# Kernel tuning notes

Hardware: AMD Instinct MI355X
Metric: run time of the kernel (lower is better)

The kernel has to match this reference:

```python
import jax, jax.numpy as jnp
import numpy as np

MEAN_STOP_TIME_S = 60.0
MIN_ROUTE_LEN = 2
DEMAND_TIME_WEIGHT = 0.5
ROUTE_TIME_WEIGHT = 0.5
UNSERVED_WEIGHT = 5.0

B, N, R, L, K = 64, 512, 40, 20, 4


def setup_inputs() -> dict:
    key = jax.random.key(0)
    ks = jax.random.split(key, 8)
    demand = jax.random.uniform(ks[0], (B, N, N), dtype=jnp.float32) * 10.0
    drive_times = jax.random.uniform(ks[1], (B, N, N), dtype=jnp.float32) * 1800.0
    transit_times = jax.random.uniform(ks[2], (B, N, N), dtype=jnp.float32) * 3600.0
    has_path = jax.random.randint(ks[3], (B, N, N), 0, 2) > 0
    n_transfers = jax.random.randint(ks[4], (B, N, N), 0, 4).astype(jnp.int32)
    # routes with -1 padding past a random per-route length
    routes = jax.random.randint(ks[5], (B, R, L), 0, N).astype(jnp.int32)
    lens = jax.random.randint(ks[6], (B, R), 0, L + 1)
    valid = jnp.arange(L)[None, None, :] < lens[:, :, None]
    batch_routes = jnp.where(valid, routes, -1)
    # per demand-edge route assignments, -1 = unused slot
    route_seqs = (jax.random.randint(ks[7], (B, N, N, K), 0, R + 1) - 1).astype(jnp.int32)
    return {
        'demand': demand, 'drive_times': drive_times, 'transit_times': transit_times,
        'has_path': has_path, 'n_transfers': n_transfers,
        'batch_routes': batch_routes, 'route_seqs': route_seqs,
    }


def _route_leg_times(batch_routes, dtm, mean_stop_time_s):
    # leg (l -> l+1) of each route: dtm[b, from, to] + stop time, masked on valid stops
    frm = batch_routes[:, :, :-1]
    to = batch_routes[:, :, 1:]
    valid = (frm >= 0) & (to >= 0)
    bidx = jnp.arange(dtm.shape[0])[:, None, None]
    times = dtm[bidx, jnp.maximum(frm, 0), jnp.maximum(to, 0)] + mean_stop_time_s
    return jnp.where(valid, times, 0.0)  # [B, R, L-1]


def _per_route_riders(demand, route_seqs, n_routes):
    # segment-sum demand over route ids; -1 slots go to a dump bucket
    def per_b(dem, rs):
        ids = rs.reshape(-1)
        vals = jnp.broadcast_to(dem[..., None], rs.shape).reshape(-1)
        ids = jnp.where(ids < 0, n_routes, ids)
        return jax.ops.segment_sum(vals, ids, num_segments=n_routes + 1)[:n_routes]
    return jax.vmap(per_b)(demand, route_seqs)  # [B, R]


def reference(demand, drive_times, transit_times, has_path, n_transfers,
              batch_routes, route_seqs):
    fdem = demand
    nopath = ~has_path
    route_lens = (batch_routes > -1).sum(-1)  # [B, R]

    n_disconnected = (nopath & (fdem > 0)).sum(axis=(1, 2))
    route_len_delta = jnp.maximum(MIN_ROUTE_LEN - route_lens, 0)
    route_len_delta = jnp.where(route_lens == 0, 0, route_len_delta)
    n_stops_oob = route_len_delta.sum(-1)  # [B]

    nt_eff = jnp.where(nopath, 3, n_transfers)
    tat = jnp.stack([
        (fdem * (nt_eff == 0)).sum(axis=(1, 2)),
        (fdem * (nt_eff == 1)).sum(axis=(1, 2)),
        (fdem * (nt_eff == 2)).sum(axis=(1, 2)),
        (fdem * (nt_eff > 2)).sum(axis=(1, 2)),
    ], axis=-1)  # trips_at_transfers [B, 4]

    trip_times = jnp.where(nopath, 0.0, transit_times)
    total_dmd_time = (fdem * trip_times).sum(axis=(1, 2))
    total_transfers = (fdem * n_transfers.astype(fdem.dtype)).sum(axis=(1, 2))
    unserved = (fdem * nopath).sum(axis=(1, 2))
    total_demand = fdem.sum(axis=(1, 2))

    leg_times = _route_leg_times(batch_routes, drive_times, MEAN_STOP_TIME_S)
    total_route_time = leg_times.sum(axis=(1, 2))
    # symmetric_routes=True: add return-direction legs
    ret = _route_leg_times(batch_routes, jnp.swapaxes(drive_times, 1, 2), MEAN_STOP_TIME_S)
    total_route_time = total_route_time + ret.sum(axis=(1, 2))

    per_route_riders = _per_route_riders(fdem, route_seqs, R)

    # cost assembly
    time_norm = drive_times.max(axis=(1, 2))
    served = total_demand - unserved
    mean_dmd_time = total_dmd_time / (served + 1e-6)
    norm_dmd_time = mean_dmd_time / time_norm
    n_routes_used = (route_lens > 0).sum(-1)
    norm_route_time = total_route_time / (time_norm * n_routes_used + 1e-6)
    n_demand_edges = (fdem > 0).sum(axis=(1, 2))
    frac_uncovered = n_disconnected / n_demand_edges
    denom = n_routes_used * MIN_ROUTE_LEN
    frac_oob = n_stops_oob / (denom + 1e-6)
    cost = (DEMAND_TIME_WEIGHT * norm_dmd_time
            + ROUTE_TIME_WEIGHT * norm_route_time
            + UNSERVED_WEIGHT * (frac_uncovered + frac_oob))
    return cost, per_route_riders, tat, total_route_time


if __name__ == '__main__':
    out = reference(**setup_inputs())
    print([o.shape for o in out])
```

## Files before the change

kernel.cpp:

```cpp
#include <hip/hip_runtime.h>

#define NB 64
#define NDIM 512
#define NNE (NDIM * NDIM)
#define NR 40
#define NL 20
#define SUBS 16
#define IT 16
#define BINS 41

#define MAIN_STRIDE 64
#define RT_OFF (NB * SUBS * MAIN_STRIDE)
#define FLAG_OFF (RT_OFF + NB * 4)

__global__ void detect_kernel(const unsigned int* __restrict__ hp, int* __restrict__ flag) {
    unsigned int v = hp[threadIdx.x];
    unsigned long long m = __ballot(v > 1u);
    if (threadIdx.x == 0) *flag = (m != 0ull) ? 1 : 0;
}

template<bool BYTE>
__device__ __forceinline__ void mloop(
    const float* __restrict__ pd, const float* __restrict__ pt,
    const float* __restrict__ pdr, const int* __restrict__ pn,
    const void* __restrict__ ph, const int* __restrict__ pr,
    float acc[10], float* __restrict__ myrow)
{
#pragma unroll 2
    for (int it = 0; it < IT; ++it) {
        const int o = it * 1024;
        const float4 dem = *(const float4*)(pd + o);
        const float4 tt  = *(const float4*)(pt + o);
        const float4 dt  = *(const float4*)(pdr + o);
        const int4   nt  = *(const int4*)(pn + o);
        const int4 r0 = *(const int4*)(pr + o * 4);
        const int4 r1 = *(const int4*)(pr + o * 4 + 4);
        const int4 r2 = *(const int4*)(pr + o * 4 + 8);
        const int4 r3 = *(const int4*)(pr + o * 4 + 12);
        int h[4];
        if (BYTE) {
            const uchar4 hb = *(const uchar4*)((const unsigned char*)ph + o);
            h[0] = hb.x; h[1] = hb.y; h[2] = hb.z; h[3] = hb.w;
        } else {
            const int4 hw = *(const int4*)((const int*)ph + o);
            h[0] = hw.x; h[1] = hw.y; h[2] = hw.z; h[3] = hw.w;
        }
        const float dm[4] = {dem.x, dem.y, dem.z, dem.w};
        const float tv[4] = {tt.x, tt.y, tt.z, tt.w};
        const float dv[4] = {dt.x, dt.y, dt.z, dt.w};
        const int   nv[4] = {nt.x, nt.y, nt.z, nt.w};
        const int4  rr[4] = {r0, r1, r2, r3};
#pragma unroll
        for (int e = 0; e < 4; ++e) {
            const float d = dm[e];
            const bool np_ = (h[e] == 0);
            const int nte = np_ ? 3 : nv[e];
            acc[0] += (nte == 0) ? d : 0.0f;
            acc[1] += (nte == 1) ? d : 0.0f;
            acc[2] += (nte == 2) ? d : 0.0f;
            acc[3] += (nte > 2) ? d : 0.0f;
            acc[4] += np_ ? 0.0f : d * tv[e];
            acc[5] += np_ ? d : 0.0f;
            acc[6] += d;
            const bool pos = d > 0.0f;
            acc[7] += (np_ && pos) ? 1.0f : 0.0f;
            acc[8] += pos ? 1.0f : 0.0f;
            acc[9] = fmaxf(acc[9], dv[e]);

            const unsigned b0 = min((unsigned)rr[e].x, (unsigned)(BINS - 1));
            const unsigned b1 = min((unsigned)rr[e].y, (unsigned)(BINS - 1));
            const unsigned b2 = min((unsigned)rr[e].z, (unsigned)(BINS - 1));
            const unsigned b3 = min((unsigned)rr[e].w, (unsigned)(BINS - 1));
            const float a0 = d;
            const float a1 = d * (1.0f + (b1 == b0));
            const float a2 = d * (1.0f + (b2 == b0) + (b2 == b1));
            const float a3 = d * (1.0f + (b3 == b0) + (b3 == b1) + (b3 == b2));
            const float v0 = myrow[b0];
            const float v1 = myrow[b1];
            const float v2 = myrow[b2];
            const float v3 = myrow[b3];
            myrow[b0] = v0 + a0;
            myrow[b1] = v1 + a1;
            myrow[b2] = v2 + a2;
            myrow[b3] = v3 + a3;
        }
    }
}

__global__ __launch_bounds__(256, 3) void main_kernel(
    const float* __restrict__ demand,
    const float* __restrict__ transit,
    const float* __restrict__ drive,
    const int* __restrict__ ntr,
    const unsigned char* __restrict__ hp_raw,
    const int* __restrict__ rseq,
    const int* __restrict__ flag,
    float* __restrict__ ws)
{
    __shared__ float bins[256 * BINS];
    __shared__ float red[4][10];
    __shared__ float red2[4][NR];
    const int tid = threadIdx.x;
    const int wave = tid >> 6, lane = tid & 63;
    float* __restrict__ myrow = bins + tid * BINS;
#pragma unroll
    for (int i = 0; i < BINS; ++i) myrow[i] = 0.0f;

    const int b = blockIdx.x >> 4, sub = blockIdx.x & 15;
    const size_t e0 = (size_t)b * NNE + (size_t)sub * (NNE / SUBS) + (size_t)tid * 4;

    float acc[10] = {0, 0, 0, 0, 0, 0, 0, 0, 0, 0};
    if (*flag != 0)
        mloop<true>(demand + e0, transit + e0, drive + e0, ntr + e0,
                    hp_raw + e0, rseq + e0 * 4, acc, myrow);
    else
        mloop<false>(demand + e0, transit + e0, drive + e0, ntr + e0,
                     ((const int*)hp_raw) + e0, rseq + e0 * 4, acc, myrow);

#pragma unroll
    for (int o = 32; o > 0; o >>= 1) {
#pragma unroll
        for (int v = 0; v < 9; ++v) acc[v] += __shfl_down(acc[v], o);
        acc[9] = fmaxf(acc[9], __shfl_down(acc[9], o));
    }
    if (lane == 0)
#pragma unroll
        for (int v = 0; v < 10; ++v) red[wave][v] = acc[v];
    __syncthreads();

    float* part = ws + (size_t)blockIdx.x * MAIN_STRIDE;
    if (tid < 10) {
        if (tid == 9)
            part[9] = fmaxf(fmaxf(red[0][9], red[1][9]), fmaxf(red[2][9], red[3][9]));
        else
            part[tid] = red[0][tid] + red[1][tid] + red[2][tid] + red[3][tid];
    }

    if (tid < 4 * NR) {
        const int g = tid / NR, j = tid - g * NR;
        float s = 0.0f;
#pragma unroll 8
        for (int r = g * 64; r < g * 64 + 64; ++r) s += bins[r * BINS + j];
        red2[g][j] = s;
    }
    __syncthreads();
    if (tid < NR)
        part[10 + tid] = red2[0][tid] + red2[1][tid] + red2[2][tid] + red2[3][tid];
}

__global__ __launch_bounds__(64) void route_kernel(
    const int* __restrict__ routes,
    const float* __restrict__ drive,
    float* __restrict__ ws)
{
    const int b = blockIdx.x;
    const int r = threadIdx.x;
    float t = 0.0f, used = 0.0f, oob = 0.0f;
    if (r < NR) {
        const int* rt = routes + (b * NR + r) * NL;
        int v[NL];
        int len = 0;
#pragma unroll
        for (int l = 0; l < NL; ++l) { v[l] = rt[l]; len += (v[l] > -1) ? 1 : 0; }
        const float* D = drive + (size_t)b * NNE;
#pragma unroll
        for (int l = 0; l < NL - 1; ++l) {
            int f = v[l], to = v[l + 1];
            if (f >= 0 && to >= 0)
                t += D[f * NDIM + to] + D[to * NDIM + f] + 120.0f;
        }
        used = (len > 0) ? 1.0f : 0.0f;
        int delta = 2 - len;
        oob = (len > 0 && delta > 0) ? (float)delta : 0.0f;
    }
#pragma unroll
    for (int o = 32; o > 0; o >>= 1) {
        t += __shfl_down(t, o);
        used += __shfl_down(used, o);
        oob += __shfl_down(oob, o);
    }
    if (r == 0) {
        float* a = ws + RT_OFF + b * 4;
        a[0] = t; a[1] = used; a[2] = oob;
    }
}

__global__ __launch_bounds__(64) void final_kernel(const float* __restrict__ ws,
                                                   float* __restrict__ out) {
    __shared__ float fin[50];
    const int b = blockIdx.x;
    const int v = threadIdx.x;
    if (v < 50) {
        const float* p = ws + (size_t)b * SUBS * MAIN_STRIDE + v;
        float a = p[0];
#pragma unroll
        for (int s = 1; s < SUBS; ++s) {
            const float x = p[(size_t)s * MAIN_STRIDE];
            a = (v == 9) ? fmaxf(a, x) : (a + x);
        }
        fin[v] = a;
    }
    __syncthreads();
    if (v == 0) {
        const float* rt = ws + RT_OFF + b * 4;
        const float trt = rt[0], nru = rt[1], noob = rt[2];
        const float dmdt = fin[4], uns = fin[5], tdem = fin[6];
        const float ndisc = fin[7], nedge = fin[8], tn = fin[9];
        const float served = tdem - uns;
        const float cost = 0.5f * ((dmdt / (served + 1e-6f)) / tn)
                         + 0.5f * (trt / (tn * nru + 1e-6f))
                         + 5.0f * (ndisc / nedge + noob / (nru * 2.0f + 1e-6f));
        out[b] = cost;
        out[64 + NB * NR + NB * 4 + b] = trt;
    }
    if (v < 4) out[64 + NB * NR + b * 4 + v] = fin[v];
    if (v >= 10 && v < 50) out[64 + b * NR + (v - 10)] = fin[v];
}

extern "C" void kernel_launch(void* const* d_in, const int* in_sizes, int n_in,
                              void* d_out, int out_size, void* d_ws, size_t ws_size,
                              hipStream_t stream) {
    const float* demand  = (const float*)d_in[0];
    const float* drive   = (const float*)d_in[1];
    const float* transit = (const float*)d_in[2];
    const unsigned char* hp = (const unsigned char*)d_in[3];
    const int* ntr    = (const int*)d_in[4];
    const int* routes = (const int*)d_in[5];
    const int* rseq   = (const int*)d_in[6];
    float* out = (float*)d_out;
    float* ws  = (float*)d_ws;
    int* flag  = (int*)(ws + FLAG_OFF);

    detect_kernel<<<1, 64, 0, stream>>>((const unsigned int*)hp, flag);
    route_kernel<<<NB, 64, 0, stream>>>(routes, drive, ws);
    main_kernel<<<NB * SUBS, 256, 0, stream>>>(demand, transit, drive, ntr, hp, rseq, flag, ws);
    final_kernel<<<NB, 64, 0, stream>>>(ws, out);
}
```

Baseline: 133.8 us.

## Software-pipeline main loop, shrink histogram LDS, merge route kernel into final

The main loop now double-buffers global loads in register structs, so the next group's loads are in flight while the current group is processed. The shared histogram drops the dump bin (40 bins instead of 41, invalid ids are weighted to zero) and occupancy is raised to 4 blocks per CU. The in-block cross-wave reductions and second barrier are removed: per-wave partials go straight to the workspace and the final kernel sums them. The route-time kernel is folded into the final kernel, saving one launch. Costs are higher register pressure from the double buffer, a 40-stride LDS layout that may raise bank conflicts, and a larger final reduction.

```diff
diff --git a/kernel.cpp b/kernel.cpp
--- a/kernel.cpp
+++ b/kernel.cpp
@@ -7,16 +7,97 @@
 #define NL 20
 #define SUBS 16
 #define IT 16
-#define BINS 41
-
-#define MAIN_STRIDE 64
-#define RT_OFF (NB * SUBS * MAIN_STRIDE)
-#define FLAG_OFF (RT_OFF + NB * 4)
+
+#define MAIN_STRIDE 256
+#define FLAG_OFF (NB * SUBS * MAIN_STRIDE)
+#define OUT_RIDERS 64
+#define OUT_TAT (64 + NB * NR)
+#define OUT_TRT (64 + NB * NR + NB * 4)
 
 __global__ void detect_kernel(const unsigned int* __restrict__ hp, int* __restrict__ flag) {
     unsigned int v = hp[threadIdx.x];
     unsigned long long m = __ballot(v > 1u);
     if (threadIdx.x == 0) *flag = (m != 0ull) ? 1 : 0;
+}
+
+struct G {
+    float4 dem, tt, dt;
+    int4 nt, r0, r1, r2, r3;
+    int h0, h1, h2, h3;
+};
+
+template<bool BYTE>
+__device__ __forceinline__ void ld(G& g,
+    const float* __restrict__ pd, const float* __restrict__ pt,
+    const float* __restrict__ pdr, const int* __restrict__ pn,
+    const void* __restrict__ ph, const int* __restrict__ pr, int o)
+{
+    g.dem = *(const float4*)(pd + o);
+    g.tt  = *(const float4*)(pt + o);
+    g.dt  = *(const float4*)(pdr + o);
+    g.nt  = *(const int4*)(pn + o);
+    g.r0  = *(const int4*)(pr + o * 4);
+    g.r1  = *(const int4*)(pr + o * 4 + 4);
+    g.r2  = *(const int4*)(pr + o * 4 + 8);
+    g.r3  = *(const int4*)(pr + o * 4 + 12);
+    if (BYTE) {
+        const uchar4 hb = *(const uchar4*)((const unsigned char*)ph + o);
+        g.h0 = hb.x; g.h1 = hb.y; g.h2 = hb.z; g.h3 = hb.w;
+    } else {
+        const int4 hw = *(const int4*)((const int*)ph + o);
+        g.h0 = hw.x; g.h1 = hw.y; g.h2 = hw.z; g.h3 = hw.w;
+    }
+}
+
+__device__ __forceinline__ void procE(float d, float ttv, float dtv, int ntv, int hv,
+                                      int i0, int i1, int i2, int i3,
+                                      float acc[10], float* __restrict__ myrow)
+{
+    const bool np_ = (hv == 0);
+    const int nte = np_ ? 3 : ntv;
+    acc[0] += (nte == 0) ? d : 0.0f;
+    acc[1] += (nte == 1) ? d : 0.0f;
+    acc[2] += (nte == 2) ? d : 0.0f;
+    acc[3] += (nte > 2) ? d : 0.0f;
+    acc[4] += np_ ? 0.0f : d * ttv;
+    acc[5] += np_ ? d : 0.0f;
+    acc[6] += d;
+    const bool pos = d > 0.0f;
+    acc[7] += (np_ && pos) ? 1.0f : 0.0f;
+    acc[8] += pos ? 1.0f : 0.0f;
+    acc[9] = fmaxf(acc[9], dtv);
+
+    const unsigned u0 = (unsigned)i0, u1 = (unsigned)i1,
+                   u2 = (unsigned)i2, u3 = (unsigned)i3;
+    const unsigned b0 = min(u0, (unsigned)(NR - 1));
+    const unsigned b1 = min(u1, (unsigned)(NR - 1));
+    const unsigned b2 = min(u2, (unsigned)(NR - 1));
+    const unsigned b3 = min(u3, (unsigned)(NR - 1));
+    const float w0 = (u0 < NR) ? d : 0.0f;
+    const float w1 = (u1 < NR) ? d : 0.0f;
+    const float w2 = (u2 < NR) ? d : 0.0f;
+    const float w3 = (u3 < NR) ? d : 0.0f;
+    const float a0 = w0;
+    const float a1 = w1 + ((b1 == b0) ? w0 : 0.0f);
+    const float a2 = w2 + ((b2 == b0) ? w0 : 0.0f) + ((b2 == b1) ? w1 : 0.0f);
+    const float a3 = w3 + ((b3 == b0) ? w0 : 0.0f) + ((b3 == b1) ? w1 : 0.0f)
+                        + ((b3 == b2) ? w2 : 0.0f);
+    const float v0 = myrow[b0];
+    const float v1 = myrow[b1];
+    const float v2 = myrow[b2];
+    const float v3 = myrow[b3];
+    myrow[b0] = v0 + a0;
+    myrow[b1] = v1 + a1;
+    myrow[b2] = v2 + a2;
+    myrow[b3] = v3 + a3;
+}
+
+__device__ __forceinline__ void procG(const G& g, float acc[10], float* __restrict__ myrow)
+{
+    procE(g.dem.x, g.tt.x, g.dt.x, g.nt.x, g.h0, g.r0.x, g.r0.y, g.r0.z, g.r0.w, acc, myrow);
+    procE(g.dem.y, g.tt.y, g.dt.y, g.nt.y, g.h1, g.r1.x, g.r1.y, g.r1.z, g.r1.w, acc, myrow);
+    procE(g.dem.z, g.tt.z, g.dt.z, g.nt.z, g.h2, g.r2.x, g.r2.y, g.r2.z, g.r2.w, acc, myrow);
+    procE(g.dem.w, g.tt.w, g.dt.w, g.nt.w, g.h3, g.r3.x, g.r3.y, g.r3.z, g.r3.w, acc, myrow);
 }
 
 template<bool BYTE>
@@ -26,68 +107,21 @@
     const void* __restrict__ ph, const int* __restrict__ pr,
     float acc[10], float* __restrict__ myrow)
 {
-#pragma unroll 2
-    for (int it = 0; it < IT; ++it) {
-        const int o = it * 1024;
-        const float4 dem = *(const float4*)(pd + o);
-        const float4 tt  = *(const float4*)(pt + o);
-        const float4 dt  = *(const float4*)(pdr + o);
-        const int4   nt  = *(const int4*)(pn + o);
-        const int4 r0 = *(const int4*)(pr + o * 4);
-        const int4 r1 = *(const int4*)(pr + o * 4 + 4);
-        const int4 r2 = *(const int4*)(pr + o * 4 + 8);
-        const int4 r3 = *(const int4*)(pr + o * 4 + 12);
-        int h[4];
-        if (BYTE) {
-            const uchar4 hb = *(const uchar4*)((const unsigned char*)ph + o);
-            h[0] = hb.x; h[1] = hb.y; h[2] = hb.z; h[3] = hb.w;
-        } else {
-            const int4 hw = *(const int4*)((const int*)ph + o);
-            h[0] = hw.x; h[1] = hw.y; h[2] = hw.z; h[3] = hw.w;
-        }
-        const float dm[4] = {dem.x, dem.y, dem.z, dem.w};
-        const float tv[4] = {tt.x, tt.y, tt.z, tt.w};
-        const float dv[4] = {dt.x, dt.y, dt.z, dt.w};
-        const int   nv[4] = {nt.x, nt.y, nt.z, nt.w};
-        const int4  rr[4] = {r0, r1, r2, r3};
-#pragma unroll
-        for (int e = 0; e < 4; ++e) {
-            const float d = dm[e];
-            const bool np_ = (h[e] == 0);
-            const int nte = np_ ? 3 : nv[e];
-            acc[0] += (nte == 0) ? d : 0.0f;
-            acc[1] += (nte == 1) ? d : 0.0f;
-            acc[2] += (nte == 2) ? d : 0.0f;
-            acc[3] += (nte > 2) ? d : 0.0f;
-            acc[4] += np_ ? 0.0f : d * tv[e];
-            acc[5] += np_ ? d : 0.0f;
-            acc[6] += d;
-            const bool pos = d > 0.0f;
-            acc[7] += (np_ && pos) ? 1.0f : 0.0f;
-            acc[8] += pos ? 1.0f : 0.0f;
-            acc[9] = fmaxf(acc[9], dv[e]);
-
-            const unsigned b0 = min((unsigned)rr[e].x, (unsigned)(BINS - 1));
-            const unsigned b1 = min((unsigned)rr[e].y, (unsigned)(BINS - 1));
-            const unsigned b2 = min((unsigned)rr[e].z, (unsigned)(BINS - 1));
-            const unsigned b3 = min((unsigned)rr[e].w, (unsigned)(BINS - 1));
-            const float a0 = d;
-            const float a1 = d * (1.0f + (b1 == b0));
-            const float a2 = d * (1.0f + (b2 == b0) + (b2 == b1));
-            const float a3 = d * (1.0f + (b3 == b0) + (b3 == b1) + (b3 == b2));
-            const float v0 = myrow[b0];
-            const float v1 = myrow[b1];
-            const float v2 = myrow[b2];
-            const float v3 = myrow[b3];
-            myrow[b0] = v0 + a0;
-            myrow[b1] = v1 + a1;
-            myrow[b2] = v2 + a2;
-            myrow[b3] = v3 + a3;
-        }
-    }
-}
-
-__global__ __launch_bounds__(256, 3) void main_kernel(
+    G A, B;
+    ld<BYTE>(A, pd, pt, pdr, pn, ph, pr, 0);
+#pragma unroll 1
+    for (int it = 0; it < IT - 2; it += 2) {
+        ld<BYTE>(B, pd, pt, pdr, pn, ph, pr, (it + 1) * 1024);
+        procG(A, acc, myrow);
+        ld<BYTE>(A, pd, pt, pdr, pn, ph, pr, (it + 2) * 1024);
+        procG(B, acc, myrow);
+    }
+    ld<BYTE>(B, pd, pt, pdr, pn, ph, pr, (IT - 1) * 1024);
+    procG(A, acc, myrow);
+    procG(B, acc, myrow);
+}
+
+__global__ __launch_bounds__(256, 4) void main_kernel(
     const float* __restrict__ demand,
     const float* __restrict__ transit,
     const float* __restrict__ drive,
@@ -97,14 +131,12 @@
     const int* __restrict__ flag,
     float* __restrict__ ws)
 {
-    __shared__ float bins[256 * BINS];
-    __shared__ float red[4][10];
-    __shared__ float red2[4][NR];
+    __shared__ float bins[256 * NR];
     const int tid = threadIdx.x;
     const int wave = tid >> 6, lane = tid & 63;
-    float* __restrict__ myrow = bins + tid * BINS;
-#pragma unroll
-    for (int i = 0; i < BINS; ++i) myrow[i] = 0.0f;
+    float* __restrict__ myrow = bins + tid * NR;
+#pragma unroll
+    for (int i = 0; i < NR; ++i) myrow[i] = 0.0f;
 
     const int b = blockIdx.x >> 4, sub = blockIdx.x & 15;
     const size_t e0 = (size_t)b * NNE + (size_t)sub * (NNE / SUBS) + (size_t)tid * 4;
@@ -123,49 +155,44 @@
         for (int v = 0; v < 9; ++v) acc[v] += __shfl_down(acc[v], o);
         acc[9] = fmaxf(acc[9], __shfl_down(acc[9], o));
     }
-    if (lane == 0)
-#pragma unroll
-        for (int v = 0; v < 10; ++v) red[wave][v] = acc[v];
+    float* part = ws + (size_t)blockIdx.x * MAIN_STRIDE;
+    if (lane == 0) {
+#pragma unroll
+        for (int v = 0; v < 10; ++v) part[wave * 10 + v] = acc[v];
+    }
     __syncthreads();
-
-    float* part = ws + (size_t)blockIdx.x * MAIN_STRIDE;
-    if (tid < 10) {
-        if (tid == 9)
-            part[9] = fmaxf(fmaxf(red[0][9], red[1][9]), fmaxf(red[2][9], red[3][9]));
-        else
-            part[tid] = red[0][tid] + red[1][tid] + red[2][tid] + red[3][tid];
-    }
 
     if (tid < 4 * NR) {
         const int g = tid / NR, j = tid - g * NR;
         float s = 0.0f;
 #pragma unroll 8
-        for (int r = g * 64; r < g * 64 + 64; ++r) s += bins[r * BINS + j];
-        red2[g][j] = s;
-    }
-    __syncthreads();
-    if (tid < NR)
-        part[10 + tid] = red2[0][tid] + red2[1][tid] + red2[2][tid] + red2[3][tid];
-}
-
-__global__ __launch_bounds__(64) void route_kernel(
+        for (int r = g * 64; r < g * 64 + 64; ++r) s += bins[r * NR + j];
+        part[40 + g * NR + j] = s;
+    }
+}
+
+__global__ __launch_bounds__(64) void final_kernel(
+    const float* __restrict__ ws,
     const int* __restrict__ routes,
     const float* __restrict__ drive,
-    float* __restrict__ ws)
-{
+    float* __restrict__ out)
+{
+    __shared__ float fin[50];
+    __shared__ float rt3[3];
     const int b = blockIdx.x;
-    const int r = threadIdx.x;
+    const int v = threadIdx.x;
+
     float t = 0.0f, used = 0.0f, oob = 0.0f;
-    if (r < NR) {
-        const int* rt = routes + (b * NR + r) * NL;
-        int v[NL];
+    if (v < NR) {
+        const int* rt = routes + (b * NR + v) * NL;
+        int rv[NL];
         int len = 0;
 #pragma unroll
-        for (int l = 0; l < NL; ++l) { v[l] = rt[l]; len += (v[l] > -1) ? 1 : 0; }
+        for (int l = 0; l < NL; ++l) { rv[l] = rt[l]; len += (rv[l] > -1) ? 1 : 0; }
         const float* D = drive + (size_t)b * NNE;
 #pragma unroll
         for (int l = 0; l < NL - 1; ++l) {
-            int f = v[l], to = v[l + 1];
+            int f = rv[l], to = rv[l + 1];
             if (f >= 0 && to >= 0)
                 t += D[f * NDIM + to] + D[to * NDIM + f] + 120.0f;
         }
@@ -179,42 +206,46 @@
         used += __shfl_down(used, o);
         oob += __shfl_down(oob, o);
     }
-    if (r == 0) {
-        float* a = ws + RT_OFF + b * 4;
-        a[0] = t; a[1] = used; a[2] = oob;
-    }
-}
-
-__global__ __launch_bounds__(64) void final_kernel(const float* __restrict__ ws,
-                                                   float* __restrict__ out) {
-    __shared__ float fin[50];
-    const int b = blockIdx.x;
-    const int v = threadIdx.x;
-    if (v < 50) {
-        const float* p = ws + (size_t)b * SUBS * MAIN_STRIDE + v;
-        float a = p[0];
-#pragma unroll
-        for (int s = 1; s < SUBS; ++s) {
-            const float x = p[(size_t)s * MAIN_STRIDE];
-            a = (v == 9) ? fmaxf(a, x) : (a + x);
+    if (v == 0) { rt3[0] = t; rt3[1] = used; rt3[2] = oob; }
+
+    const float* base = ws + (size_t)b * SUBS * MAIN_STRIDE;
+    if (v < NR) {
+        float s = 0.0f;
+#pragma unroll 4
+        for (int i = 0; i < SUBS * 4; ++i)
+            s += base[(i >> 2) * MAIN_STRIDE + 40 + (i & 3) * NR + v];
+        fin[v] = s;
+    } else if (v < 50) {
+        const int k = v - 40;
+        if (k == 9) {
+            float m = 0.0f;
+#pragma unroll 4
+            for (int i = 0; i < SUBS * 4; ++i)
+                m = fmaxf(m, base[(i >> 2) * MAIN_STRIDE + (i & 3) * 10 + 9]);
+            fin[v] = m;
+        } else {
+            float s = 0.0f;
+#pragma unroll 4
+            for (int i = 0; i < SUBS * 4; ++i)
+                s += base[(i >> 2) * MAIN_STRIDE + (i & 3) * 10 + k];
+            fin[v] = s;
         }
-        fin[v] = a;
     }
     __syncthreads();
+
     if (v == 0) {
-        const float* rt = ws + RT_OFF + b * 4;
-        const float trt = rt[0], nru = rt[1], noob = rt[2];
-        const float dmdt = fin[4], uns = fin[5], tdem = fin[6];
-        const float ndisc = fin[7], nedge = fin[8], tn = fin[9];
+        const float trt = rt3[0], nru = rt3[1], noob = rt3[2];
+        const float dmdt = fin[44], uns = fin[45], tdem = fin[46];
+        const float ndisc = fin[47], nedge = fin[48], tn = fin[49];
         const float served = tdem - uns;
         const float cost = 0.5f * ((dmdt / (served + 1e-6f)) / tn)
                          + 0.5f * (trt / (tn * nru + 1e-6f))
                          + 5.0f * (ndisc / nedge + noob / (nru * 2.0f + 1e-6f));
         out[b] = cost;
-        out[64 + NB * NR + NB * 4 + b] = trt;
-    }
-    if (v < 4) out[64 + NB * NR + b * 4 + v] = fin[v];
-    if (v >= 10 && v < 50) out[64 + b * NR + (v - 10)] = fin[v];
+        out[OUT_TRT + b] = trt;
+    }
+    if (v < NR) out[OUT_RIDERS + b * NR + v] = fin[v];
+    if (v >= 40 && v < 44) out[OUT_TAT + b * 4 + (v - 40)] = fin[v];
 }
 
 extern "C" void kernel_launch(void* const* d_in, const int* in_sizes, int n_in,
@@ -232,7 +263,6 @@
     int* flag  = (int*)(ws + FLAG_OFF);
 
     detect_kernel<<<1, 64, 0, stream>>>((const unsigned int*)hp, flag);
-    route_kernel<<<NB, 64, 0, stream>>>(routes, drive, ws);
     main_kernel<<<NB * SUBS, 256, 0, stream>>>(demand, transit, drive, ntr, hp, rseq, flag, ws);
-    final_kernel<<<NB, 64, 0, stream>>>(ws, out);
-}
+    final_kernel<<<NB, 64, 0, stream>>>(ws, routes, drive, out);
+}
```

After: 141.6 us. 1.06x slower.
